# Performance work log

Measured on AMD Instinct MI355X. Metric: run time of the kernel, lower is better.

## Reference

```python
import jax, jax.numpy as jnp
import numpy as np
import math

B, S, HID = 2, 2048, 1024
NH, HD = 16, 64
MAX_SEQ = 65536  # RoPE base from RotaryEmbedding


def _rope_tables(seq_len, dim):
    inv_freq = 1.0 / (MAX_SEQ ** (jnp.arange(0, dim, 2, dtype=jnp.float32) / dim))
    t = jnp.arange(seq_len, dtype=jnp.float32)
    freqs = jnp.einsum('i,j->ij', t, inv_freq)          # [S, dim/2]
    emb = jnp.concatenate([freqs, freqs], axis=-1)      # [S, dim]
    return jnp.cos(emb), jnp.sin(emb)


def _rotate_half(x):
    x1, x2 = jnp.split(x, 2, axis=-1)
    return jnp.concatenate([-x2, x1], axis=-1)


def setup_inputs() -> dict:
    key = jax.random.key(0)
    ks = jax.random.split(key, 9)
    std_qkv = 1.0 / math.sqrt(NH * HD)
    std_o = 1.0 / math.sqrt(HID)
    return {
        'input_embeds': jax.random.normal(ks[0], (B, S, HID), dtype=jnp.float32),
        'Wq': jax.random.normal(ks[1], (NH * HD, HID), dtype=jnp.float32) * std_qkv,
        'bq': jnp.zeros((NH * HD,), dtype=jnp.float32),
        'Wk': jax.random.normal(ks[2], (NH * HD, HID), dtype=jnp.float32) * std_qkv,
        'bk': jnp.zeros((NH * HD,), dtype=jnp.float32),
        'Wv': jax.random.normal(ks[3], (NH * HD, HID), dtype=jnp.float32) * std_qkv,
        'bv': jnp.zeros((NH * HD,), dtype=jnp.float32),
        'Wo': jax.random.normal(ks[4], (HID, NH * HD), dtype=jnp.float32) * std_o,
        'bo': jnp.zeros((HID,), dtype=jnp.float32),
    }


def reference(input_embeds, Wq, bq, Wk, bk, Wv, bv, Wo, bo):
    x = input_embeds
    b, s, _ = x.shape
    # QKV projections (torch Linear: x @ W.T + b)
    q = x @ Wq.T + bq
    k = x @ Wk.T + bk
    v = x @ Wv.T + bv
    # [B, S, NH*HD] -> [B, NH, S, HD]
    q = q.reshape(b, s, NH, HD).transpose(0, 2, 1, 3)
    k = k.reshape(b, s, NH, HD).transpose(0, 2, 1, 3)
    v = v.reshape(b, s, NH, HD).transpose(0, 2, 1, 3)
    # RoPE
    cos, sin = _rope_tables(s, HD)  # [S, HD]
    q = q * cos + _rotate_half(q) * sin
    k = k * cos + _rotate_half(k) * sin
    # SDPA (non-causal, no mask)
    scale = 1.0 / math.sqrt(HD)
    scores = jnp.einsum('bhqd,bhkd->bhqk', q, k) * scale
    attn = jax.nn.softmax(scores, axis=-1)
    out = jnp.einsum('bhqk,bhkd->bhqd', attn, v)
    # [B, NH, S, HD] -> [B, S, NH*HD]
    out = out.transpose(0, 2, 1, 3).reshape(b, s, NH * HD)
    return out @ Wo.T + bo
```

## Files before the change

### kernel.cpp

```cpp
#include <hip/hip_runtime.h>
#include <cstdint>
#include <cstddef>

#define S_LEN 2048
#define NHEAD 16
#define HDIM  64
#define HID_  1024

typedef short s8v  __attribute__((ext_vector_type(8)));
typedef short s4v  __attribute__((ext_vector_type(4)));
typedef float f4v  __attribute__((ext_vector_type(4)));
typedef float f16v __attribute__((ext_vector_type(16)));

__device__ __forceinline__ short f2b(float x) {
    union { float f; unsigned u; } a; a.f = x;
    unsigned r = a.u + 0x7fffu + ((a.u >> 16) & 1u);
    return (short)(r >> 16);
}
__device__ __forceinline__ float b2f(short x) {
    union { unsigned u; float f; } a; a.u = ((unsigned)(unsigned short)x) << 16;
    return a.f;
}

__device__ __forceinline__ void gload_lds16(const void* g, void* l) {
    __builtin_amdgcn_global_load_lds(
        (__attribute__((address_space(1))) void*)const_cast<void*>(g),
        (__attribute__((address_space(3))) void*)l, 16, 0, 0);
}

__device__ __forceinline__ unsigned cvtpk(float a, float b) {
    unsigned r;
    asm("v_cvt_pk_bf16_f32 %0, %1, %2" : "=v"(r) : "v"(a), "v"(b));
    return r;
}
__device__ __forceinline__ void plswap(unsigned& a, unsigned& b) {
    asm("v_permlane32_swap_b32 %0, %1" : "+v"(a), "+v"(b));
}

__global__ __launch_bounds__(256) void prep_kernel(
    const float* __restrict__ X,
    const float* __restrict__ Wq, const float* __restrict__ Wk,
    const float* __restrict__ Wv, const float* __restrict__ Wo,
    short* __restrict__ Xb, short* __restrict__ Wcat, short* __restrict__ Wob,
    float2* __restrict__ rtab)
{
    const int bid = blockIdx.x;
    if (bid < 8192) {
        const float* src;
        short* dst;
        int i;
        if (bid < 4096) {
            src = X; dst = Xb; i = bid * 256 + threadIdx.x;
        } else {
            int w = (bid - 4096) >> 10;
            src = (w == 0) ? Wq : (w == 1) ? Wk : (w == 2) ? Wv : Wo;
            dst = (w < 3) ? (Wcat + (size_t)w * 1048576) : Wob;
            i = ((bid - 4096) & 1023) * 256 + threadIdx.x;
        }
        float4 v = reinterpret_cast<const float4*>(src)[i];
        s4v o;
        o[0] = f2b(v.x); o[1] = f2b(v.y); o[2] = f2b(v.z); o[3] = f2b(v.w);
        reinterpret_cast<s4v*>(dst)[i] = o;
    } else {
        int idx = (bid - 8192) * 256 + threadIdx.x;
        int s = idx >> 5, j = idx & 31;
        float inv = exp2f(-0.5f * (float)j);
        float ang = (float)s * inv;
        float2 cs; cs.x = cosf(ang); cs.y = sinf(ang);
        rtab[idx] = cs;
    }
}

__global__ __launch_bounds__(256, 4) void gemm_qkv(
    const short* __restrict__ A, const short* __restrict__ Bw,
    const float* __restrict__ bq, const float* __restrict__ bk,
    const float* __restrict__ bv,
    short* __restrict__ Qo, short* __restrict__ Ko, short* __restrict__ Vo,
    const float2* __restrict__ rtab)
{
    __shared__ short Asl[128 * 32];
    __shared__ short Bsl[128 * 32];
    const int t = threadIdx.x;
    const int lane = t & 63;
    const int l15 = lane & 15, l4 = lane >> 4;
    const int wid = t >> 6;
    const int blk = blockIdx.x;
    const int x = blk & 7, j = blk >> 3;
    const int tn = (x * 3 + j % 3) * 128;
    const int tm = (j / 3) * 128;
    const int K = 1024;
    const int wrow = (wid >> 1) * 64, wcol = (wid & 1) * 64;

    f4v acc[4][4];
#pragma unroll
    for (int i = 0; i < 4; ++i)
#pragma unroll
        for (int jj = 0; jj < 4; ++jj) acc[i][jj] = (f4v){0.f, 0.f, 0.f, 0.f};

    const int r0 = t >> 2;
    const int c0 = (t & 3) * 8;

    const short* Ap0 = A  + (size_t)(tm + r0)      * K + c0;
    const short* Ap1 = A  + (size_t)(tm + 64 + r0) * K + c0;
    const short* Bp0 = Bw + (size_t)(tn + r0)      * K + c0;
    const short* Bp1 = Bw + (size_t)(tn + 64 + r0) * K + c0;
    short* wAlo = Asl + t * 8;
    short* wAhi = Asl + 2048 + t * 8;
    short* wBlo = Bsl + t * 8;
    short* wBhi = Bsl + 2048 + t * 8;

    {
        s8v ga0 = *(const s8v*)(Ap0);
        s8v ga1 = *(const s8v*)(Ap1);
        s8v gb0 = *(const s8v*)(Bp0);
        s8v gb1 = *(const s8v*)(Bp1);
        *(s8v*)wAlo = ga0; *(s8v*)wAhi = ga1;
        *(s8v*)wBlo = gb0; *(s8v*)wBhi = gb1;
    }
    __syncthreads();

    for (int kt = 0; kt < 32; ++kt) {
        s8v ga0, ga1, gb0, gb1;
        const bool pre = (kt < 31);
        if (pre) {
            const int k0 = (kt + 1) << 5;
            ga0 = *(const s8v*)(Ap0 + k0);
            ga1 = *(const s8v*)(Ap1 + k0);
            gb0 = *(const s8v*)(Bp0 + k0);
            gb1 = *(const s8v*)(Bp1 + k0);
        }
        s8v af[4], bf[4];
#pragma unroll
        for (int i = 0; i < 4; ++i) {
            af[i] = *(const s8v*)&Asl[(wrow + i * 16 + l15) * 32 + 8 * l4];
            bf[i] = *(const s8v*)&Bsl[(wcol + i * 16 + l15) * 32 + 8 * l4];
        }
#pragma unroll
        for (int i = 0; i < 4; ++i)
#pragma unroll
            for (int jj = 0; jj < 4; ++jj)
                acc[i][jj] = __builtin_amdgcn_mfma_f32_16x16x32_bf16(af[i], bf[jj], acc[i][jj], 0, 0, 0);
        __syncthreads();
        if (pre) {
            *(s8v*)wAlo = ga0; *(s8v*)wAhi = ga1;
            *(s8v*)wBlo = gb0; *(s8v*)wBhi = gb1;
        }
        __syncthreads();
    }

    const int mode = tn >> 10;
    const float* bias = (mode == 0) ? bq : (mode == 1) ? bk : bv;
    short* outb = (mode == 0) ? Qo : (mode == 1) ? Ko : Vo;

    if (mode == 2) {
#pragma unroll
        for (int i = 0; i < 4; ++i) {
            int rowb = tm + wrow + i * 16 + l4 * 4;
            int b_ = rowb >> 11, s0 = rowb & 2047;
#pragma unroll
            for (int jj = 0; jj < 4; ++jj) {
                int col = tn + wcol + jj * 16 + l15;
                int cm = col & 1023;
                float bvv = bias[cm];
                int h = cm >> 6, d = col & 63;
                s4v o4;
#pragma unroll
                for (int r = 0; r < 4; ++r) o4[r] = f2b(acc[i][jj][r] + bvv);
                *(s4v*)&outb[((size_t)((b_ * NHEAD + h) * 64 + d)) * S_LEN + s0] = o4;
            }
        }
    } else {
        int h = ((tn & 1023) + wcol) >> 6;
        const float osc = (mode == 0) ? 0.180336880111f : 1.0f;
#pragma unroll
        for (int i = 0; i < 4; ++i) {
#pragma unroll
            for (int r = 0; r < 4; ++r) {
                int row = tm + wrow + i * 16 + l4 * 4 + r;
                int b_ = row >> 11, s = row & 2047;
                float2 cs0 = rtab[(s << 5) + l15];
                float2 cs1 = rtab[(s << 5) + 16 + l15];
#pragma unroll
                for (int jj = 0; jj < 4; ++jj) {
                    int col = tn + wcol + jj * 16 + l15;
                    int cm = col & 1023;
                    int d = col & 63;
                    float v  = acc[i][jj][r]     + bias[cm];
                    float vp = acc[i][jj ^ 2][r] + bias[cm ^ 32];
                    float2 cs = (jj & 1) ? cs1 : cs0;
                    float res = (d < 32) ? (v * cs.x - vp * cs.y)
                                         : (v * cs.x + vp * cs.y);
                    outb[(((size_t)(b_ * NHEAD + h) * S_LEN + s) << 6) + d] = f2b(res * osc);
                }
            }
        }
    }
}

__global__ __launch_bounds__(256) void gemm_o(
    const short* __restrict__ A, const short* __restrict__ Bw,
    const float* __restrict__ bias, float* __restrict__ outf)
{
    __shared__ short Asl[2][64 * 32];
    __shared__ short Bsl[2][128 * 32];
    const int t = threadIdx.x;
    const int lane = t & 63;
    const int l15 = lane & 15, l4 = lane >> 4;
    const int wid = t >> 6;
    const int blk = blockIdx.x;
    const int tn = (blk & 7) * 128;
    const int tm = (blk >> 3) * 64;
    const int K = 1024, N = 1024;
    const int wrow = (wid >> 1) * 32, wcol = (wid & 1) * 64;

    f4v acc[2][4];
#pragma unroll
    for (int i = 0; i < 2; ++i)
#pragma unroll
        for (int jj = 0; jj < 4; ++jj) acc[i][jj] = (f4v){0.f, 0.f, 0.f, 0.f};

    const int r0 = t >> 2;
    const int c0 = (t & 3) * 8;
    const int wbase = (t & ~63) * 8;

#define OSTAGE(buf, kt) do { const int k0_ = (kt) << 5;                            \
        gload_lds16(A  + (size_t)(tm + r0)      * K + k0_ + c0, &Asl[buf][wbase]);        \
        gload_lds16(Bw + (size_t)(tn + r0)      * K + k0_ + c0, &Bsl[buf][wbase]);        \
        gload_lds16(Bw + (size_t)(tn + 64 + r0) * K + k0_ + c0, &Bsl[buf][2048 + wbase]); \
    } while (0)

    OSTAGE(0, 0);
    int cur = 0;
    for (int kt = 0; kt < 32; ++kt) {
        if (kt < 31) {
            OSTAGE(cur ^ 1, kt + 1);
            asm volatile("s_waitcnt vmcnt(3)" ::: "memory");
        } else {
            asm volatile("s_waitcnt vmcnt(0)" ::: "memory");
        }
        __builtin_amdgcn_s_barrier();
        __builtin_amdgcn_sched_barrier(0);
        s8v af[2], bf[4];
#pragma unroll
        for (int i = 0; i < 2; ++i)
            af[i] = *(const s8v*)&Asl[cur][(wrow + i * 16 + l15) * 32 + 8 * l4];
#pragma unroll
        for (int jj = 0; jj < 4; ++jj)
            bf[jj] = *(const s8v*)&Bsl[cur][(wcol + jj * 16 + l15) * 32 + 8 * l4];
#pragma unroll
        for (int i = 0; i < 2; ++i)
#pragma unroll
            for (int jj = 0; jj < 4; ++jj)
                acc[i][jj] = __builtin_amdgcn_mfma_f32_16x16x32_bf16(af[i], bf[jj], acc[i][jj], 0, 0, 0);
        __builtin_amdgcn_s_barrier();
        cur ^= 1;
    }
#undef OSTAGE

#pragma unroll
    for (int i = 0; i < 2; ++i) {
        int rowb = tm + wrow + i * 16 + l4 * 4;
#pragma unroll
        for (int jj = 0; jj < 4; ++jj) {
            int col = tn + wcol + jj * 16 + l15;
            float bv = bias[col];
#pragma unroll
            for (int r = 0; r < 4; ++r)
                outf[(size_t)(rowb + r) * N + col] = acc[i][jj][r] + bv;
        }
    }
}

#define SWB(row, bofs) ((bofs) ^ (((row) & 7) << 4))

__global__ __launch_bounds__(256, 4) void attn_split(
    const short* __restrict__ Q, const short* __restrict__ K,
    const short* __restrict__ Vt,
    short* __restrict__ P0, short* __restrict__ P1, float2* __restrict__ ML)
{
    __shared__ short Kl[4096];
    __shared__ short Vl[4096];

    const int t = threadIdx.x, lane = t & 63;
    const int wid = t >> 6;
    const int q5 = lane & 31, hi = lane >> 5;

    const int blk = blockIdx.x;
    const int x = blk & 7, j = blk >> 3;
    const int bh = x * 4 + (j & 3);
    const int rest = j >> 2;
    const int qb = rest & 15, split = rest >> 4;
    const int kt0 = split * 16;

    const short* Qb = Q + (size_t)bh * S_LEN * 64;
    const char*  Kb = (const char*)(K  + (size_t)bh * S_LEN * 64);
    const char*  Vb = (const char*)(Vt + (size_t)bh * S_LEN * 64);
    const int qrow = qb * 128 + wid * 32 + q5;

    s8v qf[4];
#pragma unroll
    for (int sl = 0; sl < 4; ++sl)
        qf[sl] = *(const s8v*)&Qb[(size_t)qrow * 64 + sl * 16 + hi * 8];

    f16v oacc[2];
#pragma unroll
    for (int dt = 0; dt < 2; ++dt)
#pragma unroll
        for (int e = 0; e < 16; ++e) oacc[dt][e] = 0.f;
    float m2 = -1e30f, lsum = 0.f;

    const int skey  = t >> 3;
    const int sboff = (t & 7) * 16;
    const int sw    = SWB(skey, sboff);
    const size_t kgoff = (size_t)skey * 128  + sboff;
    const size_t vgoff = (size_t)skey * 4096 + sboff;
    char* KlB = (char*)Kl;
    char* VlB = (char*)Vl;
    const int w0 = skey * 128 + sw;
    const int w1 = w0 + 32 * 128;

    {
        const size_t kbB = (size_t)kt0 * 64 * 128;
        const size_t vbB = (size_t)kt0 * 64 * 2;
        s8v g0 = *(const s8v*)(Kb + kbB + kgoff);
        s8v g1 = *(const s8v*)(Kb + kbB + kgoff + 32 * 128);
        s8v g2 = *(const s8v*)(Vb + vbB + vgoff);
        s8v g3 = *(const s8v*)(Vb + vbB + vgoff + 32 * 4096);
        *(s8v*)(KlB + w0) = g0; *(s8v*)(KlB + w1) = g1;
        *(s8v*)(VlB + w0) = g2; *(s8v*)(VlB + w1) = g3;
    }
    __syncthreads();

    for (int kt = kt0; kt < kt0 + 16; ++kt) {
        s8v g0, g1, g2, g3;
        const bool pre = (kt < kt0 + 15);
        if (pre) {
            const size_t kbB = (size_t)(kt + 1) * 64 * 128;
            const size_t vbB = (size_t)(kt + 1) * 64 * 2;
            g0 = *(const s8v*)(Kb + kbB + kgoff);
            g1 = *(const s8v*)(Kb + kbB + kgoff + 32 * 128);
            g2 = *(const s8v*)(Vb + vbB + vgoff);
            g3 = *(const s8v*)(Vb + vbB + vgoff + 32 * 4096);
        }

        f16v sc[2];
#pragma unroll
        for (int e = 0; e < 16; ++e) { sc[0][e] = 0.f; sc[1][e] = 0.f; }
        {
            const int kr0 = q5, kr1 = 32 + q5;
            const char* kb0 = KlB + kr0 * 128;
            const char* kb1 = KlB + kr1 * 128;
            __builtin_amdgcn_s_setprio(1);
#pragma unroll
            for (int sl = 0; sl < 4; ++sl) {
                s8v kf0 = *(const s8v*)(kb0 + SWB(kr0, sl * 32 + hi * 16));
                s8v kf1 = *(const s8v*)(kb1 + SWB(kr1, sl * 32 + hi * 16));
                sc[0] = __builtin_amdgcn_mfma_f32_32x32x16_bf16(kf0, qf[sl], sc[0], 0, 0, 0);
                sc[1] = __builtin_amdgcn_mfma_f32_32x32x16_bf16(kf1, qf[sl], sc[1], 0, 0, 0);
            }
            __builtin_amdgcn_s_setprio(0);
        }

        float m8[8];
#pragma unroll
        for (int e = 0; e < 8; ++e)
            m8[e] = fmaxf(fmaxf(sc[0][e], sc[0][e + 8]), fmaxf(sc[1][e], sc[1][e + 8]));
        float pm = fmaxf(fmaxf(fmaxf(m8[0], m8[4]), fmaxf(m8[1], m8[5])),
                         fmaxf(fmaxf(m8[2], m8[6]), fmaxf(m8[3], m8[7])));
        pm = fmaxf(pm, __shfl_xor(pm, 32, 64));
        if (__any(pm > m2 + 8.0f)) {
            float m2n = fmaxf(m2, pm);
            float fr = __builtin_amdgcn_exp2f(m2 - m2n);
            lsum *= fr;
#pragma unroll
            for (int dt = 0; dt < 2; ++dt)
#pragma unroll
                for (int e = 0; e < 16; ++e) oacc[dt][e] *= fr;
            m2 = m2n;
        }
#pragma unroll
        for (int c = 0; c < 2; ++c)
#pragma unroll
            for (int e = 0; e < 16; ++e)
                sc[c][e] = __builtin_amdgcn_exp2f(sc[c][e] - m2);
        float sum8[8];
#pragma unroll
        for (int e = 0; e < 8; ++e)
            sum8[e] = (sc[0][e] + sc[0][e + 8]) + (sc[1][e] + sc[1][e + 8]);
        lsum += ((sum8[0] + sum8[4]) + (sum8[1] + sum8[5])) +
                ((sum8[2] + sum8[6]) + (sum8[3] + sum8[7]));

#pragma unroll
        for (int c = 0; c < 2; ++c) {
#pragma unroll
            for (int ks = 0; ks < 2; ++ks) {
                const int b0 = ks * 8;
                unsigned x0 = cvtpk(sc[c][b0 + 0], sc[c][b0 + 1]);
                unsigned y0 = cvtpk(sc[c][b0 + 4], sc[c][b0 + 5]);
                unsigned x1 = cvtpk(sc[c][b0 + 2], sc[c][b0 + 3]);
                unsigned y1 = cvtpk(sc[c][b0 + 6], sc[c][b0 + 7]);
                plswap(x0, y0);
                plswap(x1, y1);
                union { unsigned u[4]; s8v s; } pf;
                pf.u[0] = x0; pf.u[1] = x1; pf.u[2] = y0; pf.u[3] = y1;
                __builtin_amdgcn_s_setprio(1);
#pragma unroll
                for (int dt = 0; dt < 2; ++dt) {
                    const int vrow = dt * 32 + q5;
                    s8v vf = *(const s8v*)(VlB + vrow * 128 +
                                           SWB(vrow, c * 64 + ks * 32 + hi * 16));
                    oacc[dt] = __builtin_amdgcn_mfma_f32_32x32x16_bf16(vf, pf.s, oacc[dt], 0, 0, 0);
                }
                __builtin_amdgcn_s_setprio(0);
            }
        }

        __syncthreads();
        if (pre) {
            *(s8v*)(KlB + w0) = g0; *(s8v*)(KlB + w1) = g1;
            *(s8v*)(VlB + w0) = g2; *(s8v*)(VlB + w1) = g3;
        }
        __syncthreads();
    }

    float ls = lsum + __shfl_xor(lsum, 32, 64);
    float inv = 1.0f / ls;
    short* Pp = (split ? P1 : P0) + ((size_t)bh * S_LEN + qrow) * 64;
#pragma unroll
    for (int dt = 0; dt < 2; ++dt)
#pragma unroll
        for (int g = 0; g < 4; ++g) {
            s4v o4;
#pragma unroll
            for (int jj = 0; jj < 4; ++jj) o4[jj] = f2b(oacc[dt][g * 4 + jj] * inv);
            const int d0 = dt * 32 + g * 8 + hi * 4;
            *(s4v*)&Pp[d0] = o4;
        }
    if (hi == 0) {
        float2 ml; ml.x = m2; ml.y = ls;
        ML[(size_t)split * (32 * S_LEN) + bh * S_LEN + qrow] = ml;
    }
}

__global__ __launch_bounds__(256) void attn_combine(
    const short* __restrict__ P0, const short* __restrict__ P1,
    const float2* __restrict__ ML, short* __restrict__ Obf)
{
    int idx = blockIdx.x * 256 + threadIdx.x;
    int row = idx >> 3;
    int d0 = (idx & 7) * 8;
    float2 a = ML[row];
    float2 b = ML[32 * S_LEN + row];
    float m = fmaxf(a.x, b.x);
    float w0 = a.y * exp2f(a.x - m);
    float w1 = b.y * exp2f(b.x - m);
    float inv = 1.0f / (w0 + w1);
    w0 *= inv; w1 *= inv;
    s8v v0 = *(const s8v*)&P0[(size_t)row * 64 + d0];
    s8v v1 = *(const s8v*)&P1[(size_t)row * 64 + d0];
    s8v o;
#pragma unroll
    for (int e = 0; e < 8; ++e) o[e] = f2b(w0 * b2f(v0[e]) + w1 * b2f(v1[e]));
    int bh = row >> 11, s = row & 2047;
    int b_ = bh >> 4, h = bh & 15;
    *(s8v*)&Obf[((size_t)(b_ * S_LEN + s)) * HID_ + h * 64 + d0] = o;
}

extern "C" void kernel_launch(void* const* d_in, const int* in_sizes, int n_in,
                              void* d_out, int out_size, void* d_ws, size_t ws_size,
                              hipStream_t stream)
{
    const float* X  = (const float*)d_in[0];
    const float* Wq = (const float*)d_in[1];
    const float* bq = (const float*)d_in[2];
    const float* Wk = (const float*)d_in[3];
    const float* bk = (const float*)d_in[4];
    const float* Wv = (const float*)d_in[5];
    const float* bv = (const float*)d_in[6];
    const float* Wo = (const float*)d_in[7];
    const float* bo = (const float*)d_in[8];
    float* out = (float*)d_out;

    char* ws = (char*)d_ws;
    short*  Xb   = (short*) (ws);
    short*  Wcat = (short*) (ws + ( 8u << 20));
    short*  Wob  = (short*) (ws + (14u << 20));
    float2* rtab = (float2*)(ws + (16u << 20));
    short*  Qbh  = (short*) (ws + (17u << 20));
    short*  Kbh  = (short*) (ws + (25u << 20));
    short*  Vbh  = (short*) (ws + (33u << 20));
    short*  Obf  = (short*) (ws + (41u << 20));
    short*  P0   = (short*) (ws);
    short*  P1   = (short*) d_out;
    float2* ML   = (float2*)((char*)d_out + (8u << 20));

    prep_kernel<<<8448, 256, 0, stream>>>(X, Wq, Wk, Wv, Wo, Xb, Wcat, Wob, rtab);
    gemm_qkv<<<768, 256, 0, stream>>>(Xb, Wcat, bq, bk, bv, Qbh, Kbh, Vbh, rtab);
    attn_split<<<1024, 256, 0, stream>>>(Qbh, Kbh, Vbh, P0, P1, ML);
    attn_combine<<<2048, 256, 0, stream>>>(P0, P1, ML, Obf);
    gemm_o<<<512, 256, 0, stream>>>(Obf, Wob, bo, out);
}
```

Measured before the change: 136.1 us.

## Fuse attention split-combine into output projection GEMM A-tile load

Removes the separate attn_combine kernel. gemm_o now reads the two partial attention outputs and their max/sum statistics directly, merges them in registers and writes the bf16 A tile to LDS. The async global_load_lds double buffer is replaced by a register prefetch of the next tile into a single LDS buffer with two barriers per iteration. This saves one launch and the Obf round trip through memory. In exchange, each A element's combine is recomputed by every N-tile block, and the main loop loses its async double buffering. Workspace buffers are moved so P1 and ML no longer live in the output buffer.

```diff
diff --git a/kernel.cpp b/kernel.cpp
--- a/kernel.cpp
+++ b/kernel.cpp
@@ -20,12 +20,6 @@
 __device__ __forceinline__ float b2f(short x) {
     union { unsigned u; float f; } a; a.u = ((unsigned)(unsigned short)x) << 16;
     return a.f;
-}
-
-__device__ __forceinline__ void gload_lds16(const void* g, void* l) {
-    __builtin_amdgcn_global_load_lds(
-        (__attribute__((address_space(1))) void*)const_cast<void*>(g),
-        (__attribute__((address_space(3))) void*)l, 16, 0, 0);
 }
 
 __device__ __forceinline__ unsigned cvtpk(float a, float b) {
@@ -197,12 +191,14 @@
     }
 }
 
-__global__ __launch_bounds__(256) void gemm_o(
-    const short* __restrict__ A, const short* __restrict__ Bw,
-    const float* __restrict__ bias, float* __restrict__ outf)
+__global__ __launch_bounds__(256, 4) void gemm_o(
+    const short* __restrict__ P0, const short* __restrict__ P1,
+    const float2* __restrict__ ML,
+    const short* __restrict__ Bw, const float* __restrict__ bias,
+    float* __restrict__ outf)
 {
-    __shared__ short Asl[2][64 * 32];
-    __shared__ short Bsl[2][128 * 32];
+    __shared__ short Asl[64 * 32];
+    __shared__ short Bsl[128 * 32];
     const int t = threadIdx.x;
     const int lane = t & 63;
     const int l15 = lane & 15, l4 = lane >> 4;
@@ -221,41 +217,78 @@
 
     const int r0 = t >> 2;
     const int c0 = (t & 3) * 8;
-    const int wbase = (t & ~63) * 8;
-
-#define OSTAGE(buf, kt) do { const int k0_ = (kt) << 5;                            \
-        gload_lds16(A  + (size_t)(tm + r0)      * K + k0_ + c0, &Asl[buf][wbase]);        \
-        gload_lds16(Bw + (size_t)(tn + r0)      * K + k0_ + c0, &Bsl[buf][wbase]);        \
-        gload_lds16(Bw + (size_t)(tn + 64 + r0) * K + k0_ + c0, &Bsl[buf][2048 + wbase]); \
+    const int grow = tm + r0;
+    const int b_ = grow >> 11, s = grow & 2047;
+
+    const short* Bp0 = Bw + (size_t)(tn + r0)      * K + c0;
+    const short* Bp1 = Bw + (size_t)(tn + 64 + r0) * K + c0;
+    short* wA   = Asl + t * 8;
+    short* wBlo = Bsl + t * 8;
+    short* wBhi = Bsl + 2048 + t * 8;
+
+#define AFETCH(kt, v0_, v1_, mA_, mB_) do {                                   \
+        int col_ = ((kt) << 5) + c0;                                          \
+        int bh_ = b_ * NHEAD + (col_ >> 6);                                   \
+        size_t pidx_ = ((size_t)bh_ * S_LEN + s) * 64 + (col_ & 63);          \
+        v0_ = *(const s8v*)&P0[pidx_];                                        \
+        v1_ = *(const s8v*)&P1[pidx_];                                        \
+        mA_ = ML[bh_ * S_LEN + s];                                            \
+        mB_ = ML[32 * S_LEN + bh_ * S_LEN + s];                               \
     } while (0)
 
-    OSTAGE(0, 0);
-    int cur = 0;
+#define ACOMBINE(v0_, v1_, mA_, mB_) do {                                     \
+        float mm_ = fmaxf(mA_.x, mB_.x);                                      \
+        float w0_ = mA_.y * exp2f(mA_.x - mm_);                               \
+        float w1_ = mB_.y * exp2f(mB_.x - mm_);                               \
+        float inv_ = 1.0f / (w0_ + w1_);                                      \
+        w0_ *= inv_; w1_ *= inv_;                                             \
+        s8v o_;                                                               \
+        _Pragma("unroll")                                                     \
+        for (int e_ = 0; e_ < 8; ++e_)                                        \
+            o_[e_] = f2b(w0_ * b2f(v0_[e_]) + w1_ * b2f(v1_[e_]));            \
+        *(s8v*)wA = o_;                                                       \
+    } while (0)
+
+    {
+        s8v v0, v1; float2 mA, mB;
+        AFETCH(0, v0, v1, mA, mB);
+        s8v gb0 = *(const s8v*)(Bp0);
+        s8v gb1 = *(const s8v*)(Bp1);
+        ACOMBINE(v0, v1, mA, mB);
+        *(s8v*)wBlo = gb0; *(s8v*)wBhi = gb1;
+    }
+    __syncthreads();
+
     for (int kt = 0; kt < 32; ++kt) {
-        if (kt < 31) {
-            OSTAGE(cur ^ 1, kt + 1);
-            asm volatile("s_waitcnt vmcnt(3)" ::: "memory");
-        } else {
-            asm volatile("s_waitcnt vmcnt(0)" ::: "memory");
-        }
-        __builtin_amdgcn_s_barrier();
-        __builtin_amdgcn_sched_barrier(0);
+        s8v v0, v1, gb0, gb1; float2 mA, mB;
+        const bool pre = (kt < 31);
+        if (pre) {
+            AFETCH(kt + 1, v0, v1, mA, mB);
+            const int k0 = (kt + 1) << 5;
+            gb0 = *(const s8v*)(Bp0 + k0);
+            gb1 = *(const s8v*)(Bp1 + k0);
+        }
         s8v af[2], bf[4];
 #pragma unroll
         for (int i = 0; i < 2; ++i)
-            af[i] = *(const s8v*)&Asl[cur][(wrow + i * 16 + l15) * 32 + 8 * l4];
+            af[i] = *(const s8v*)&Asl[(wrow + i * 16 + l15) * 32 + 8 * l4];
 #pragma unroll
         for (int jj = 0; jj < 4; ++jj)
-            bf[jj] = *(const s8v*)&Bsl[cur][(wcol + jj * 16 + l15) * 32 + 8 * l4];
+            bf[jj] = *(const s8v*)&Bsl[(wcol + jj * 16 + l15) * 32 + 8 * l4];
 #pragma unroll
         for (int i = 0; i < 2; ++i)
 #pragma unroll
             for (int jj = 0; jj < 4; ++jj)
                 acc[i][jj] = __builtin_amdgcn_mfma_f32_16x16x32_bf16(af[i], bf[jj], acc[i][jj], 0, 0, 0);
-        __builtin_amdgcn_s_barrier();
-        cur ^= 1;
-    }
-#undef OSTAGE
+        __syncthreads();
+        if (pre) {
+            ACOMBINE(v0, v1, mA, mB);
+            *(s8v*)wBlo = gb0; *(s8v*)wBhi = gb1;
+        }
+        __syncthreads();
+    }
+#undef AFETCH
+#undef ACOMBINE
 
 #pragma unroll
     for (int i = 0; i < 2; ++i) {
@@ -440,30 +473,6 @@
         float2 ml; ml.x = m2; ml.y = ls;
         ML[(size_t)split * (32 * S_LEN) + bh * S_LEN + qrow] = ml;
     }
-}
-
-__global__ __launch_bounds__(256) void attn_combine(
-    const short* __restrict__ P0, const short* __restrict__ P1,
-    const float2* __restrict__ ML, short* __restrict__ Obf)
-{
-    int idx = blockIdx.x * 256 + threadIdx.x;
-    int row = idx >> 3;
-    int d0 = (idx & 7) * 8;
-    float2 a = ML[row];
-    float2 b = ML[32 * S_LEN + row];
-    float m = fmaxf(a.x, b.x);
-    float w0 = a.y * exp2f(a.x - m);
-    float w1 = b.y * exp2f(b.x - m);
-    float inv = 1.0f / (w0 + w1);
-    w0 *= inv; w1 *= inv;
-    s8v v0 = *(const s8v*)&P0[(size_t)row * 64 + d0];
-    s8v v1 = *(const s8v*)&P1[(size_t)row * 64 + d0];
-    s8v o;
-#pragma unroll
-    for (int e = 0; e < 8; ++e) o[e] = f2b(w0 * b2f(v0[e]) + w1 * b2f(v1[e]));
-    int bh = row >> 11, s = row & 2047;
-    int b_ = bh >> 4, h = bh & 15;
-    *(s8v*)&Obf[((size_t)(b_ * S_LEN + s)) * HID_ + h * 64 + d0] = o;
 }
 
 extern "C" void kernel_launch(void* const* d_in, const int* in_sizes, int n_in,
@@ -489,14 +498,12 @@
     short*  Qbh  = (short*) (ws + (17u << 20));
     short*  Kbh  = (short*) (ws + (25u << 20));
     short*  Vbh  = (short*) (ws + (33u << 20));
-    short*  Obf  = (short*) (ws + (41u << 20));
     short*  P0   = (short*) (ws);
-    short*  P1   = (short*) d_out;
-    float2* ML   = (float2*)((char*)d_out + (8u << 20));
+    short*  P1   = (short*) (ws + (41u << 20));
+    float2* ML   = (float2*)(ws + (16u << 20));
 
     prep_kernel<<<8448, 256, 0, stream>>>(X, Wq, Wk, Wv, Wo, Xb, Wcat, Wob, rtab);
     gemm_qkv<<<768, 256, 0, stream>>>(Xb, Wcat, bq, bk, bv, Qbh, Kbh, Vbh, rtab);
     attn_split<<<1024, 256, 0, stream>>>(Qbh, Kbh, Vbh, P0, P1, ML);
-    attn_combine<<<2048, 256, 0, stream>>>(P0, P1, ML, Obf);
-    gemm_o<<<512, 256, 0, stream>>>(Obf, Wob, bo, out);
-}
+    gemm_o<<<512, 256, 0, stream>>>(P0, P1, ML, Wob, bo, out);
+}
```

After: 142.1 us. 1.04x slower.
